# Performance work log

Hardware: AMD Instinct MI355X
Metric: run time of the kernel (lower is better)

Reference implementation:

```python
import jax, jax.numpy as jnp
import numpy as np

B, HT, WD, DIM = 8, 128, 128, 512
NUM_HEADS = 8
HEAD_DIM = DIM // NUM_HEADS
K = 7  # kernel_size
R = K // 2


def setup_inputs() -> dict:
    key = jax.random.key(0)
    k1, k2 = jax.random.split(key)
    x = jax.random.normal(k1, (B, HT, WD, DIM), dtype=jnp.float32)
    # nn.Linear(dim, 2*dim, bias=False); stored as [in, out] so y = x @ W_qk
    W_qk = jax.random.normal(k2, (DIM, 2 * DIM), dtype=jnp.float32) * (DIM ** -0.5)
    return {"x": x, "W_qk": W_qk}


def reference(x, W_qk):
    Bsz, H, W, C = x.shape
    scale = HEAD_DIM ** -0.5
    # qk projection -> [B,H,W,2,heads,head_dim]
    qk = (x @ W_qk).reshape(Bsz, H, W, 2, NUM_HEADS, HEAD_DIM)
    q = qk[..., 0, :, :] * scale          # [B,H,W,hd,d]
    kk = qk[..., 1, :, :]                 # [B,H,W,hd,d]
    # NATTEN border handling: window start clamped so the KxK window stays inside.
    starts_i = jnp.clip(jnp.arange(H) - R, 0, H - K)  # [H]
    starts_j = jnp.clip(jnp.arange(W) - R, 0, W - K)  # [W]
    attn = []
    for ki in range(K):
        k_row = kk[:, starts_i + ki]          # [B,H,W,hd,d] (gather rows)
        for kj in range(K):
            k_n = k_row[:, :, starts_j + kj]  # [B,H,W,hd,d] (gather cols)
            attn.append(jnp.einsum('bhwnd,bhwnd->bhwn', q, k_n))
    attn = jnp.stack(attn, axis=-1)           # [B,H,W,hd,K*K]
    return jnp.transpose(attn, (0, 3, 1, 2, 4))  # [B,hd,H,W,K*K]
```

## Files before the change

### kernel.cpp

```cpp
#include <hip/hip_runtime.h>

typedef __attribute__((ext_vector_type(8))) short short8;
typedef __attribute__((ext_vector_type(4))) float floatx4;

__device__ __forceinline__ unsigned short f2bf(float f) {
  union { float f; unsigned u; } x; x.f = f;
  unsigned u = x.u + 0x7fffu + ((x.u >> 16) & 1u);
  return (unsigned short)(u >> 16);
}

__device__ __forceinline__ void gload_lds16(const void* g, void* l) {
  __builtin_amdgcn_global_load_lds(
      (const __attribute__((address_space(1))) unsigned int*)g,
      (__attribute__((address_space(3))) unsigned int*)l, 16, 0, 0);
}


__global__ __launch_bounds__(256) void cvt_x(const float4* __restrict__ x,
                                             uint2* __restrict__ o) {
  size_t idx = (size_t)blockIdx.x * 256 + threadIdx.x;
  float4 v = x[idx];
  uint2 r;
  r.x = (unsigned)f2bf(v.x) | ((unsigned)f2bf(v.y) << 16);
  r.y = (unsigned)f2bf(v.z) | ((unsigned)f2bf(v.w) << 16);
  o[idx] = r;
}

__global__ __launch_bounds__(256) void cvt_w(const float* __restrict__ w,
                                             unsigned short* __restrict__ wt) {
  int tid = blockIdx.x * 256 + threadIdx.x;
  int n = tid >> 9, k = tid & 511;
  float v = w[k * 1024 + n];
  if (n < 512) v *= 0.125f;
  wt[tid] = f2bf(v);
}

__global__ __launch_bounds__(512, 2) void gemm_bt(const unsigned short* __restrict__ A,
                                                  const unsigned short* __restrict__ Bt,
                                                  unsigned short* __restrict__ C) {
  __shared__ __align__(16) unsigned short lds_a[4][4 * 256 * 8];
  __shared__ __align__(16) unsigned short lds_b[4][4 * 256 * 8];

  const int t = threadIdx.x;
  const int bid = blockIdx.x;
  const int wg = (bid & 7) * 256 + (bid >> 3);
  const int mtile = wg >> 2;
  const int ntile = wg & 3;
  const int m0 = mtile * 256, n0 = ntile * 256;
  const int wave = t >> 6, lane = t & 63;
  const int wm = (wave >> 2) * 128, wn = (wave & 3) * 64;
  const int kg = lane >> 4, rr = lane & 15;

  const unsigned short* aP[2];
  const unsigned short* bP[2];
#pragma unroll
  for (int p = 0; p < 2; ++p) {
    int S = t + p * 512, kgrp = S >> 8, row = S & 255;
    aP[p] = &A[(size_t)(m0 + row) * 512 + kgrp * 8];
    bP[p] = &Bt[(size_t)(n0 + row) * 512 + kgrp * 8];
  }

#pragma unroll
  for (int tt = 0; tt < 3; ++tt) {
#pragma unroll
    for (int p = 0; p < 2; ++p) {
      gload_lds16(aP[p] + tt * 32, &lds_a[tt][(t + p * 512) * 8]);
      gload_lds16(bP[p] + tt * 32, &lds_b[tt][(t + p * 512) * 8]);
    }
  }

  floatx4 acc[8][4] = {};

#pragma unroll
  for (int step = 0; step < 16; ++step) {
    if (step < 14)
      asm volatile("s_waitcnt vmcnt(8)\n\ts_barrier" ::: "memory");
    else if (step == 14)
      asm volatile("s_waitcnt vmcnt(4)\n\ts_barrier" ::: "memory");
    else
      asm volatile("s_waitcnt vmcnt(0)\n\ts_barrier" ::: "memory");

    if (step + 3 < 16) {
      const int k0n = (step + 3) * 32;
      const int nb = (step + 3) & 3;
#pragma unroll
      for (int p = 0; p < 2; ++p) {
        gload_lds16(aP[p] + k0n, &lds_a[nb][(t + p * 512) * 8]);
        gload_lds16(bP[p] + k0n, &lds_b[nb][(t + p * 512) * 8]);
      }
    }

    const int cur = step & 3;
    short8 af[8], bf[4];
#pragma unroll
    for (int i = 0; i < 8; ++i)
      af[i] = *(const short8*)&lds_a[cur][(kg * 256 + wm + i * 16 + rr) * 8];
#pragma unroll
    for (int j = 0; j < 4; ++j)
      bf[j] = *(const short8*)&lds_b[cur][(kg * 256 + wn + j * 16 + rr) * 8];
    __builtin_amdgcn_s_setprio(1);
#pragma unroll
    for (int i = 0; i < 8; ++i)
#pragma unroll
      for (int j = 0; j < 4; ++j)
        acc[i][j] = __builtin_amdgcn_mfma_f32_16x16x32_bf16(af[i], bf[j], acc[i][j], 0, 0, 0);
    __builtin_amdgcn_s_setprio(0);
  }

  __syncthreads();
  unsigned short* creg = (wave < 4) ? &lds_a[wave][0] : &lds_b[wave - 4][0];
#pragma unroll
  for (int i = 0; i < 8; ++i)
#pragma unroll
    for (int j = 0; j < 4; ++j)
#pragma unroll
      for (int r = 0; r < 4; ++r)
        creg[(i * 16 + kg * 4 + r) * 64 + j * 16 + rr] = f2bf(acc[i][j][r]);
  asm volatile("s_waitcnt lgkmcnt(0)" ::: "memory");
  {
    unsigned short* Cg = C + (size_t)(m0 + wm) * 1024 + n0 + wn;
#pragma unroll
    for (int p = 0; p < 16; ++p) {
      int idx = p * 64 + lane;
      int row = idx >> 3, cg8 = idx & 7;
      uint4 v = *(const uint4*)&creg[row * 64 + cg8 * 8];
      *(uint4*)&Cg[(size_t)row * 1024 + cg8 * 8] = v;
    }
  }
}

__global__ __launch_bounds__(256) void attn_mfma(const unsigned short* __restrict__ QK,
                                                 float* __restrict__ out) {
  __shared__ __align__(16) unsigned short q_lds[128 * 64];
  __shared__ __align__(16) unsigned short k_lds[2][128 * 64];
  __shared__ __align__(16) float s_scr[4][24 * 20];
  __shared__ __align__(16) float out_lds[128 * 49];

  const int t = threadIdx.x;
  const int bid = blockIdx.x;
  const int wg = (bid & 7) * 1024 + (bid >> 3);
  const int i = wg & 127;
  const int h = (wg >> 7) & 7;
  const int b = wg >> 10;
  const int wave = t >> 6, lane = t & 63;
  const int kg = lane >> 4, rr = lane & 15;
  const int ri = min(max(i - 3, 0), 121);

  const unsigned short* qbase = QK + ((size_t)(b * 128 + i) * 128) * 1024 + h * 64;
#pragma unroll
  for (int s = 0; s < 4; ++s) {
    int S = t + s * 256;
    int j = S >> 3, pg = S & 7, lg = pg ^ (j & 7);
    gload_lds16(qbase + (size_t)j * 1024 + lg * 8, &q_lds[S * 8]);
  }
#pragma unroll
  for (int kt = 0; kt < 2; ++kt) {
    const unsigned short* kb = QK + ((size_t)(b * 128 + ri + kt) * 128) * 1024 + 512 + h * 64;
#pragma unroll
    for (int s = 0; s < 4; ++s) {
      int S = t + s * 256;
      int c = S >> 3, pg = S & 7, lg = pg ^ (c & 7);
      gload_lds16(kb + (size_t)c * 1024 + lg * 8, &k_lds[kt][S * 8]);
    }
  }

  asm volatile("s_waitcnt vmcnt(8)\n\ts_barrier" ::: "memory");

  short8 af[2][2];
#pragma unroll
  for (int jt2 = 0; jt2 < 2; ++jt2) {
    int row = (wave * 2 + jt2) * 16 + rr;
#pragma unroll
    for (int ks = 0; ks < 2; ++ks) {
      int lg = ks * 4 + kg;
      af[jt2][ks] = *(const short8*)&q_lds[(row * 8 + (lg ^ (row & 7))) * 8];
    }
  }

  const int m = lane >> 2, kj0 = lane & 3;

#pragma unroll
  for (int ki = 0; ki < 7; ++ki) {
    if (ki < 6)
      asm volatile("s_waitcnt vmcnt(4)\n\ts_barrier" ::: "memory");
    else
      asm volatile("s_waitcnt vmcnt(0)\n\ts_barrier" ::: "memory");

    const unsigned short* kbuf = k_lds[ki & 1];
    float* scr = s_scr[wave];

#pragma unroll
    for (int jt2 = 0; jt2 < 2; ++jt2) {
      const int j0 = (wave * 2 + jt2) * 16;
      const int cb = min(max(j0 - 3, 0), 121);
      const int c0 = min(cb + rr, 127);
      const int c1 = min(cb + 16 + rr, 127);
      floatx4 acc0 = {0.f, 0.f, 0.f, 0.f}, acc1 = {0.f, 0.f, 0.f, 0.f};
      __builtin_amdgcn_s_setprio(1);
#pragma unroll
      for (int ks = 0; ks < 2; ++ks) {
        int lg = ks * 4 + kg;
        short8 b0 = *(const short8*)&kbuf[(c0 * 8 + (lg ^ (c0 & 7))) * 8];
        short8 b1 = *(const short8*)&kbuf[(c1 * 8 + (lg ^ (c1 & 7))) * 8];
        acc0 = __builtin_amdgcn_mfma_f32_16x16x32_bf16(af[jt2][ks], b0, acc0, 0, 0, 0);
        acc1 = __builtin_amdgcn_mfma_f32_16x16x32_bf16(af[jt2][ks], b1, acc1, 0, 0, 0);
      }
      __builtin_amdgcn_s_setprio(0);
      {
        int crow = (lane >> 4) * 4;
        *(floatx4*)&scr[rr * 20 + crow] = acc0;
        if (rr < 8) *(floatx4*)&scr[(16 + rr) * 20 + crow] = acc1;
      }
      asm volatile("s_waitcnt lgkmcnt(0)" ::: "memory");
      {
        int relc = min(max(j0 + m - 3, 0), 121) - cb;
        int p = j0 + m;
        out_lds[p * 49 + ki * 7 + kj0] = scr[(relc + kj0) * 20 + m];
        if (kj0 < 3)
          out_lds[p * 49 + ki * 7 + 4 + kj0] = scr[(relc + 4 + kj0) * 20 + m];
      }
      asm volatile("s_waitcnt lgkmcnt(0)" ::: "memory");
    }

    asm volatile("s_barrier" ::: "memory");
    if (ki + 2 <= 6) {
      const unsigned short* kb =
          QK + ((size_t)(b * 128 + ri + ki + 2) * 128) * 1024 + 512 + h * 64;
#pragma unroll
      for (int s = 0; s < 4; ++s) {
        int S = t + s * 256;
        int c = S >> 3, pg = S & 7, lg = pg ^ (c & 7);
        gload_lds16(kb + (size_t)c * 1024 + lg * 8, &k_lds[ki & 1][S * 8]);
      }
    }
  }

  const uint4* src = (const uint4*)out_lds;
  uint4* dst = (uint4*)(out + ((size_t)(b * 8 + h) * 16384 + (size_t)i * 128) * 49);
  for (int s = t; s < 1568; s += 256) dst[s] = src[s];
}

extern "C" void kernel_launch(void* const* d_in, const int* in_sizes, int n_in,
                              void* d_out, int out_size, void* d_ws, size_t ws_size,
                              hipStream_t stream) {
  const float* x = (const float*)d_in[0];
  const float* w = (const float*)d_in[1];
  float* out = (float*)d_out;

  unsigned short* xb = (unsigned short*)d_ws;
  unsigned short* wt = xb + 67108864;
  unsigned short* qk = wt + 524288;

  cvt_x<<<65536, 256, 0, stream>>>((const float4*)x, (uint2*)xb);
  cvt_w<<<2048, 256, 0, stream>>>(w, wt);
  gemm_bt<<<2048, 512, 0, stream>>>(xb, wt, qk);
  attn_mfma<<<8192, 256, 0, stream>>>(qk, out);
}
```

Baseline: 859.0 us.

## Restructure QK GEMM to keep full weight tile in LDS and stream A from global

The projection GEMM now loads a full 64-column by 512-K slice of the weight matrix into swizzled LDS once. Each wave then reads its A rows directly from global memory into registers per k-step, replacing the multi-stage LDS double-buffered pipeline with barriers. This removes per-step synchronisation and A staging, but reloads A from global/L2 for every one of the 16 N tiles and drops explicit prefetching, so memory latency may be exposed.

```diff
diff --git a/kernel.cpp b/kernel.cpp
--- a/kernel.cpp
+++ b/kernel.cpp
@@ -35,96 +35,68 @@
   wt[tid] = f2bf(v);
 }
 
-__global__ __launch_bounds__(512, 2) void gemm_bt(const unsigned short* __restrict__ A,
+__global__ __launch_bounds__(256, 2) void gemm_bt(const unsigned short* __restrict__ A,
                                                   const unsigned short* __restrict__ Bt,
                                                   unsigned short* __restrict__ C) {
-  __shared__ __align__(16) unsigned short lds_a[4][4 * 256 * 8];
-  __shared__ __align__(16) unsigned short lds_b[4][4 * 256 * 8];
+  __shared__ __align__(16) unsigned short B_lds[64 * 512];
 
   const int t = threadIdx.x;
   const int bid = blockIdx.x;
-  const int wg = (bid & 7) * 256 + (bid >> 3);
-  const int mtile = wg >> 2;
-  const int ntile = wg & 3;
-  const int m0 = mtile * 256, n0 = ntile * 256;
+  const int wg = (bid & 7) * 512 + (bid >> 3);
+  const int mp = wg >> 4;
+  const int nt = wg & 15;
+  const int m0 = mp * 512, n0 = nt * 64;
   const int wave = t >> 6, lane = t & 63;
-  const int wm = (wave >> 2) * 128, wn = (wave & 3) * 64;
   const int kg = lane >> 4, rr = lane & 15;
 
-  const unsigned short* aP[2];
-  const unsigned short* bP[2];
-#pragma unroll
-  for (int p = 0; p < 2; ++p) {
-    int S = t + p * 512, kgrp = S >> 8, row = S & 255;
-    aP[p] = &A[(size_t)(m0 + row) * 512 + kgrp * 8];
-    bP[p] = &Bt[(size_t)(n0 + row) * 512 + kgrp * 8];
-  }
-
-#pragma unroll
-  for (int tt = 0; tt < 3; ++tt) {
-#pragma unroll
-    for (int p = 0; p < 2; ++p) {
-      gload_lds16(aP[p] + tt * 32, &lds_a[tt][(t + p * 512) * 8]);
-      gload_lds16(bP[p] + tt * 32, &lds_b[tt][(t + p * 512) * 8]);
-    }
-  }
+#pragma unroll
+  for (int s = 0; s < 16; ++s) {
+    int S = t + s * 256;
+    int c = S >> 6, g = S & 63, gs = g ^ (c & 7);
+    gload_lds16(&Bt[(size_t)(n0 + c) * 512 + gs * 8], &B_lds[S * 8]);
+  }
+  __syncthreads();
+
+  const unsigned short* Abase = A + (size_t)(m0 + wave * 128 + rr) * 512 + kg * 8;
 
   floatx4 acc[8][4] = {};
-
-#pragma unroll
-  for (int step = 0; step < 16; ++step) {
-    if (step < 14)
-      asm volatile("s_waitcnt vmcnt(8)\n\ts_barrier" ::: "memory");
-    else if (step == 14)
-      asm volatile("s_waitcnt vmcnt(4)\n\ts_barrier" ::: "memory");
-    else
-      asm volatile("s_waitcnt vmcnt(0)\n\ts_barrier" ::: "memory");
-
-    if (step + 3 < 16) {
-      const int k0n = (step + 3) * 32;
-      const int nb = (step + 3) & 3;
-#pragma unroll
-      for (int p = 0; p < 2; ++p) {
-        gload_lds16(aP[p] + k0n, &lds_a[nb][(t + p * 512) * 8]);
-        gload_lds16(bP[p] + k0n, &lds_b[nb][(t + p * 512) * 8]);
-      }
-    }
-
-    const int cur = step & 3;
-    short8 af[8], bf[4];
+#pragma unroll 2
+  for (int kc = 0; kc < 16; ++kc) {
+    short8 af[8];
 #pragma unroll
     for (int i = 0; i < 8; ++i)
-      af[i] = *(const short8*)&lds_a[cur][(kg * 256 + wm + i * 16 + rr) * 8];
-#pragma unroll
-    for (int j = 0; j < 4; ++j)
-      bf[j] = *(const short8*)&lds_b[cur][(kg * 256 + wn + j * 16 + rr) * 8];
-    __builtin_amdgcn_s_setprio(1);
+      af[i] = *(const short8*)(Abase + (size_t)i * 16 * 512 + kc * 32);
+    short8 bf[4];
+#pragma unroll
+    for (int j = 0; j < 4; ++j) {
+      int c = j * 16 + rr;
+      bf[j] = *(const short8*)&B_lds[c * 512 + ((kc * 4 + kg) ^ (c & 7)) * 8];
+    }
 #pragma unroll
     for (int i = 0; i < 8; ++i)
 #pragma unroll
       for (int j = 0; j < 4; ++j)
         acc[i][j] = __builtin_amdgcn_mfma_f32_16x16x32_bf16(af[i], bf[j], acc[i][j], 0, 0, 0);
-    __builtin_amdgcn_s_setprio(0);
   }
 
   __syncthreads();
-  unsigned short* creg = (wave < 4) ? &lds_a[wave][0] : &lds_b[wave - 4][0];
+  unsigned short* cst = &B_lds[wave * 8192];
 #pragma unroll
   for (int i = 0; i < 8; ++i)
 #pragma unroll
     for (int j = 0; j < 4; ++j)
 #pragma unroll
       for (int r = 0; r < 4; ++r)
-        creg[(i * 16 + kg * 4 + r) * 64 + j * 16 + rr] = f2bf(acc[i][j][r]);
+        cst[(i * 16 + kg * 4 + r) * 64 + j * 16 + rr] = f2bf(acc[i][j][r]);
   asm volatile("s_waitcnt lgkmcnt(0)" ::: "memory");
   {
-    unsigned short* Cg = C + (size_t)(m0 + wm) * 1024 + n0 + wn;
+    unsigned short* Cg = C + (size_t)(m0 + wave * 128) * 1024 + n0;
 #pragma unroll
     for (int p = 0; p < 16; ++p) {
       int idx = p * 64 + lane;
-      int row = idx >> 3, cg8 = idx & 7;
-      uint4 v = *(const uint4*)&creg[row * 64 + cg8 * 8];
-      *(uint4*)&Cg[(size_t)row * 1024 + cg8 * 8] = v;
+      int lr = idx >> 3, g8 = idx & 7;
+      uint4 v = *(const uint4*)&cst[lr * 64 + g8 * 8];
+      *(uint4*)&Cg[(size_t)lr * 1024 + g8 * 8] = v;
     }
   }
 }
@@ -253,6 +225,6 @@
 
   cvt_x<<<65536, 256, 0, stream>>>((const float4*)x, (uint2*)xb);
   cvt_w<<<2048, 256, 0, stream>>>(w, wt);
-  gemm_bt<<<2048, 512, 0, stream>>>(xb, wt, qk);
+  gemm_bt<<<4096, 256, 0, stream>>>(xb, wt, qk);
   attn_mfma<<<8192, 256, 0, stream>>>(qk, out);
 }
```

Measured after the change: 907.9 us. 5.7% more time.

## Split GEMM k-step into two MFMA phases and scatter attention scores directly

Applied to the files above, without the earlier changes.

The GEMM main loop now splits each k-step into two halves. A-tile prefetches are issued with the first half's B fragments and B-tile prefetches with the second half, and extra barriers separate each phase. This interleaves global-to-LDS loads with MFMA work and lowers register pressure, at the cost of more barriers. The attention kernel drops its per-wave scratch buffer and writes the MFMA accumulator lanes straight into the output LDS tile with a bounds check, removing one LDS round trip and two waitcnts per tile. A final __syncthreads is added before the output copy.

```diff
diff --git a/kernel.cpp b/kernel.cpp
--- a/kernel.cpp
+++ b/kernel.cpp
@@ -38,8 +38,8 @@
 __global__ __launch_bounds__(512, 2) void gemm_bt(const unsigned short* __restrict__ A,
                                                   const unsigned short* __restrict__ Bt,
                                                   unsigned short* __restrict__ C) {
-  __shared__ __align__(16) unsigned short lds_a[4][4 * 256 * 8];
-  __shared__ __align__(16) unsigned short lds_b[4][4 * 256 * 8];
+  __shared__ __align__(16) unsigned short lds_a[4][8192];
+  __shared__ __align__(16) unsigned short lds_b[4][8192];
 
   const int t = threadIdx.x;
   const int bid = blockIdx.x;
@@ -48,83 +48,97 @@
   const int ntile = wg & 3;
   const int m0 = mtile * 256, n0 = ntile * 256;
   const int wave = t >> 6, lane = t & 63;
-  const int wm = (wave >> 2) * 128, wn = (wave & 3) * 64;
+  const int wr = wave >> 2, wc = wave & 3;
   const int kg = lane >> 4, rr = lane & 15;
 
   const unsigned short* aP[2];
   const unsigned short* bP[2];
 #pragma unroll
-  for (int p = 0; p < 2; ++p) {
-    int S = t + p * 512, kgrp = S >> 8, row = S & 255;
-    aP[p] = &A[(size_t)(m0 + row) * 512 + kgrp * 8];
-    bP[p] = &Bt[(size_t)(n0 + row) * 512 + kgrp * 8];
-  }
-
-#pragma unroll
-  for (int tt = 0; tt < 3; ++tt) {
-#pragma unroll
-    for (int p = 0; p < 2; ++p) {
-      gload_lds16(aP[p] + tt * 32, &lds_a[tt][(t + p * 512) * 8]);
-      gload_lds16(bP[p] + tt * 32, &lds_b[tt][(t + p * 512) * 8]);
-    }
-  }
+  for (int l = 0; l < 2; ++l) {
+    int S = t + l * 512, kgrp = S >> 8, row = S & 255;
+    aP[l] = &A[(size_t)(m0 + row) * 512 + kgrp * 8];
+    bP[l] = &Bt[(size_t)(n0 + row) * 512 + kgrp * 8];
+  }
+
+#pragma unroll
+  for (int tt = 0; tt < 3; ++tt)
+#pragma unroll
+    for (int l = 0; l < 2; ++l) {
+      gload_lds16(aP[l] + tt * 32, &lds_a[tt][(t + l * 512) * 8]);
+      gload_lds16(bP[l] + tt * 32, &lds_b[tt][(t + l * 512) * 8]);
+    }
 
   floatx4 acc[8][4] = {};
 
 #pragma unroll
-  for (int step = 0; step < 16; ++step) {
-    if (step < 14)
+  for (int kt = 0; kt < 16; ++kt) {
+    const int cur = kt & 3;
+    if (kt <= 13)
       asm volatile("s_waitcnt vmcnt(8)\n\ts_barrier" ::: "memory");
-    else if (step == 14)
+    else if (kt == 14)
       asm volatile("s_waitcnt vmcnt(4)\n\ts_barrier" ::: "memory");
     else
       asm volatile("s_waitcnt vmcnt(0)\n\ts_barrier" ::: "memory");
 
-    if (step + 3 < 16) {
-      const int k0n = (step + 3) * 32;
-      const int nb = (step + 3) & 3;
-#pragma unroll
-      for (int p = 0; p < 2; ++p) {
-        gload_lds16(aP[p] + k0n, &lds_a[nb][(t + p * 512) * 8]);
-        gload_lds16(bP[p] + k0n, &lds_b[nb][(t + p * 512) * 8]);
-      }
-    }
-
-    const int cur = step & 3;
-    short8 af[8], bf[4];
+    short8 af[8];
 #pragma unroll
     for (int i = 0; i < 8; ++i)
-      af[i] = *(const short8*)&lds_a[cur][(kg * 256 + wm + i * 16 + rr) * 8];
+      af[i] = *(const short8*)&lds_a[cur][(kg * 256 + wr * 128 + i * 16 + rr) * 8];
+    short8 b0 = *(const short8*)&lds_b[cur][(kg * 256 + wc * 64 + 0 * 16 + rr) * 8];
+    short8 b1 = *(const short8*)&lds_b[cur][(kg * 256 + wc * 64 + 1 * 16 + rr) * 8];
+    if (kt <= 12) {
+      const int nb = (kt + 3) & 3, k0n = (kt + 3) * 32;
+#pragma unroll
+      for (int l = 0; l < 2; ++l)
+        gload_lds16(aP[l] + k0n, &lds_a[nb][(t + l * 512) * 8]);
+    }
+    asm volatile("s_barrier" ::: "memory");
+    __builtin_amdgcn_s_setprio(1);
+#pragma unroll
+    for (int i = 0; i < 8; ++i) {
+      acc[i][0] = __builtin_amdgcn_mfma_f32_16x16x32_bf16(af[i], b0, acc[i][0], 0, 0, 0);
+      acc[i][1] = __builtin_amdgcn_mfma_f32_16x16x32_bf16(af[i], b1, acc[i][1], 0, 0, 0);
+    }
+    __builtin_amdgcn_s_setprio(0);
+    asm volatile("s_barrier" ::: "memory");
+
+    short8 b2 = *(const short8*)&lds_b[cur][(kg * 256 + wc * 64 + 2 * 16 + rr) * 8];
+    short8 b3 = *(const short8*)&lds_b[cur][(kg * 256 + wc * 64 + 3 * 16 + rr) * 8];
+    if (kt <= 12) {
+      const int nb = (kt + 3) & 3, k0n = (kt + 3) * 32;
+#pragma unroll
+      for (int l = 0; l < 2; ++l)
+        gload_lds16(bP[l] + k0n, &lds_b[nb][(t + l * 512) * 8]);
+    }
+    asm volatile("s_barrier" ::: "memory");
+    __builtin_amdgcn_s_setprio(1);
+#pragma unroll
+    for (int i = 0; i < 8; ++i) {
+      acc[i][2] = __builtin_amdgcn_mfma_f32_16x16x32_bf16(af[i], b2, acc[i][2], 0, 0, 0);
+      acc[i][3] = __builtin_amdgcn_mfma_f32_16x16x32_bf16(af[i], b3, acc[i][3], 0, 0, 0);
+    }
+    __builtin_amdgcn_s_setprio(0);
+    asm volatile("s_barrier" ::: "memory");
+  }
+
+  __syncthreads();
+  unsigned short* cst = (wave < 4) ? &lds_a[wave][0] : &lds_b[wave - 4][0];
+#pragma unroll
+  for (int i = 0; i < 8; ++i)
 #pragma unroll
     for (int j = 0; j < 4; ++j)
-      bf[j] = *(const short8*)&lds_b[cur][(kg * 256 + wn + j * 16 + rr) * 8];
-    __builtin_amdgcn_s_setprio(1);
-#pragma unroll
-    for (int i = 0; i < 8; ++i)
-#pragma unroll
-      for (int j = 0; j < 4; ++j)
-        acc[i][j] = __builtin_amdgcn_mfma_f32_16x16x32_bf16(af[i], bf[j], acc[i][j], 0, 0, 0);
-    __builtin_amdgcn_s_setprio(0);
-  }
-
-  __syncthreads();
-  unsigned short* creg = (wave < 4) ? &lds_a[wave][0] : &lds_b[wave - 4][0];
-#pragma unroll
-  for (int i = 0; i < 8; ++i)
-#pragma unroll
-    for (int j = 0; j < 4; ++j)
 #pragma unroll
       for (int r = 0; r < 4; ++r)
-        creg[(i * 16 + kg * 4 + r) * 64 + j * 16 + rr] = f2bf(acc[i][j][r]);
+        cst[(i * 16 + kg * 4 + r) * 64 + j * 16 + rr] = f2bf(acc[i][j][r]);
   asm volatile("s_waitcnt lgkmcnt(0)" ::: "memory");
   {
-    unsigned short* Cg = C + (size_t)(m0 + wm) * 1024 + n0 + wn;
+    unsigned short* Cg = C + (size_t)(m0 + wr * 128) * 1024 + n0 + wc * 64;
 #pragma unroll
     for (int p = 0; p < 16; ++p) {
       int idx = p * 64 + lane;
-      int row = idx >> 3, cg8 = idx & 7;
-      uint4 v = *(const uint4*)&creg[row * 64 + cg8 * 8];
-      *(uint4*)&Cg[(size_t)row * 1024 + cg8 * 8] = v;
+      int lr = idx >> 3, g8 = idx & 7;
+      uint4 v = *(const uint4*)&cst[lr * 64 + g8 * 8];
+      *(uint4*)&Cg[(size_t)lr * 1024 + g8 * 8] = v;
     }
   }
 }
@@ -133,7 +147,6 @@
                                                  float* __restrict__ out) {
   __shared__ __align__(16) unsigned short q_lds[128 * 64];
   __shared__ __align__(16) unsigned short k_lds[2][128 * 64];
-  __shared__ __align__(16) float s_scr[4][24 * 20];
   __shared__ __align__(16) float out_lds[128 * 49];
 
   const int t = threadIdx.x;
@@ -177,8 +190,6 @@
     }
   }
 
-  const int m = lane >> 2, kj0 = lane & 3;
-
 #pragma unroll
   for (int ki = 0; ki < 7; ++ki) {
     if (ki < 6)
@@ -187,7 +198,6 @@
       asm volatile("s_waitcnt vmcnt(0)\n\ts_barrier" ::: "memory");
 
     const unsigned short* kbuf = k_lds[ki & 1];
-    float* scr = s_scr[wave];
 
 #pragma unroll
     for (int jt2 = 0; jt2 < 2; ++jt2) {
@@ -206,20 +216,15 @@
         acc1 = __builtin_amdgcn_mfma_f32_16x16x32_bf16(af[jt2][ks], b1, acc1, 0, 0, 0);
       }
       __builtin_amdgcn_s_setprio(0);
-      {
-        int crow = (lane >> 4) * 4;
-        *(floatx4*)&scr[rr * 20 + crow] = acc0;
-        if (rr < 8) *(floatx4*)&scr[(16 + rr) * 20 + crow] = acc1;
+#pragma unroll
+      for (int r = 0; r < 4; ++r) {
+        int p = j0 + kg * 4 + r;
+        int relc = min(max(p - 3, 0), 121) - cb;
+        int k0a = rr - relc;
+        if ((unsigned)k0a < 7u) out_lds[p * 49 + ki * 7 + k0a] = acc0[r];
+        int k1a = 16 + rr - relc;
+        if ((unsigned)k1a < 7u) out_lds[p * 49 + ki * 7 + k1a] = acc1[r];
       }
-      asm volatile("s_waitcnt lgkmcnt(0)" ::: "memory");
-      {
-        int relc = min(max(j0 + m - 3, 0), 121) - cb;
-        int p = j0 + m;
-        out_lds[p * 49 + ki * 7 + kj0] = scr[(relc + kj0) * 20 + m];
-        if (kj0 < 3)
-          out_lds[p * 49 + ki * 7 + 4 + kj0] = scr[(relc + 4 + kj0) * 20 + m];
-      }
-      asm volatile("s_waitcnt lgkmcnt(0)" ::: "memory");
     }
 
     asm volatile("s_barrier" ::: "memory");
@@ -235,6 +240,7 @@
     }
   }
 
+  __syncthreads();
   const uint4* src = (const uint4*)out_lds;
   uint4* dst = (uint4*)(out + ((size_t)(b * 8 + h) * 16384 + (size_t)i * 128) * 49);
   for (int s = t; s < 1568; s += 256) dst[s] = src[s];
```

New measurement: 811.6 us. 1.06x faster.
